# Optimization experiments

Measured on AMD Instinct MI355X. Metric: run time of the kernel, lower is better.

Reference implementation:

```python
import itertools
import jax, jax.numpy as jnp
import numpy as np

TAU = 1e-06


def build_A_system(M: int) -> np.ndarray:
    """All binary matrices A in {0,1}^{2 x M} with exactly one 1 per column,
    excluding the two assignments where one group is empty. Shape [K, 2, M],
    K = 2^M - 2."""
    mats = []
    for assign in itertools.product([0, 1], repeat=M):
        s = sum(assign)
        if s == 0 or s == M:
            continue
        A = np.zeros((2, M), dtype=np.float32)
        for i, val in enumerate(assign):
            A[val, i] = 1.0
        mats.append(A)
    return np.stack(mats, axis=0)


def setup_inputs() -> dict:
    key = jax.random.key(0)
    k1, k2 = jax.random.split(key)
    B, M, T = 8, 8, 32000
    estimated_sources = jax.random.normal(k1, (B, M, T), dtype=jnp.float32)
    input_mixtures = jax.random.normal(k2, (B, 2, T), dtype=jnp.float32)
    return {"estimated_sources": estimated_sources, "input_mixtures": input_mixtures}


def reference(estimated_sources, input_mixtures):
    B, M, T = estimated_sources.shape
    assert input_mixtures.shape[1] == 2
    # [K, 2, M] binary assignment matrices (static, built at trace time)
    A = jnp.asarray(build_A_system(M), dtype=estimated_sources.dtype)
    # Remix estimated sources under every assignment: [B, K, 2, T]
    est = jnp.einsum('kjm,bmt->bkjt', A, estimated_sources)
    # Per-mixture input energy: [B, 2]
    input_energy = jnp.sum(input_mixtures ** 2, axis=-1)
    # Noise energy per (batch, combo, mixture): [B, K, 2]
    noise_energy = jnp.sum((input_mixtures[:, None, :, :] - est) ** 2, axis=-1)
    ie = input_energy[:, None, :]  # [B, 1, 2] broadcast over K
    # Negative SNR in dB: [B, K, 2]
    snr_loss = -10.0 * jnp.log10(ie / (noise_energy + TAU * ie))
    # Sum over the two mixtures, minimize over assignments, mean over batch
    per_combo = jnp.sum(snr_loss, axis=-1)     # [B, K]
    per_sample = jnp.min(per_combo, axis=-1)   # [B]
    return jnp.mean(per_sample)
```

## Files before the change

kernel.cpp:

```cpp
#include <hip/hip_runtime.h>
#include <math.h>

#define TAU 1e-6f

constexpr int Mm = 8;
constexpr int Bb = 8;
constexpr int Tt = 32000;
constexpr int NCOL = Tt / 4;
constexpr int BLKS_PER_B = 32;
constexpr int NBLK = BLKS_PER_B * Bb;
constexpr int NSTAT = 54;
constexpr int WS_STRIDE = 64;

#define STAT_LIST(X) \
  X(e0,0) X(e1,1) \
  X(c00,2) X(c01,3) X(c02,4) X(c03,5) X(c04,6) X(c05,7) X(c06,8) X(c07,9) \
  X(c10,10) X(c11,11) X(c12,12) X(c13,13) X(c14,14) X(c15,15) X(c16,16) X(c17,17) \
  X(g00,18) X(g01,19) X(g02,20) X(g03,21) X(g04,22) X(g05,23) X(g06,24) X(g07,25) \
  X(g11,26) X(g12,27) X(g13,28) X(g14,29) X(g15,30) X(g16,31) X(g17,32) \
  X(g22,33) X(g23,34) X(g24,35) X(g25,36) X(g26,37) X(g27,38) \
  X(g33,39) X(g34,40) X(g35,41) X(g36,42) X(g37,43) \
  X(g44,44) X(g45,45) X(g46,46) X(g47,47) \
  X(g55,48) X(g56,49) X(g57,50) \
  X(g66,51) X(g67,52) \
  X(g77,53)

#define DECL_STAT(v,i) float v = 0.0f;

#define COMP_UPDATE(F) do { \
  const float x0 = x0v.F, x1 = x1v.F; \
  const float t0 = s0v.F, t1 = s1v.F, t2 = s2v.F, t3 = s3v.F; \
  const float t4 = s4v.F, t5 = s5v.F, t6 = s6v.F, t7 = s7v.F; \
  e0 = fmaf(x0, x0, e0);  e1 = fmaf(x1, x1, e1); \
  c00 = fmaf(x0, t0, c00); c01 = fmaf(x0, t1, c01); c02 = fmaf(x0, t2, c02); c03 = fmaf(x0, t3, c03); \
  c04 = fmaf(x0, t4, c04); c05 = fmaf(x0, t5, c05); c06 = fmaf(x0, t6, c06); c07 = fmaf(x0, t7, c07); \
  c10 = fmaf(x1, t0, c10); c11 = fmaf(x1, t1, c11); c12 = fmaf(x1, t2, c12); c13 = fmaf(x1, t3, c13); \
  c14 = fmaf(x1, t4, c14); c15 = fmaf(x1, t5, c15); c16 = fmaf(x1, t6, c16); c17 = fmaf(x1, t7, c17); \
  g00 = fmaf(t0, t0, g00); g01 = fmaf(t0, t1, g01); g02 = fmaf(t0, t2, g02); g03 = fmaf(t0, t3, g03); \
  g04 = fmaf(t0, t4, g04); g05 = fmaf(t0, t5, g05); g06 = fmaf(t0, t6, g06); g07 = fmaf(t0, t7, g07); \
  g11 = fmaf(t1, t1, g11); g12 = fmaf(t1, t2, g12); g13 = fmaf(t1, t3, g13); g14 = fmaf(t1, t4, g14); \
  g15 = fmaf(t1, t5, g15); g16 = fmaf(t1, t6, g16); g17 = fmaf(t1, t7, g17); \
  g22 = fmaf(t2, t2, g22); g23 = fmaf(t2, t3, g23); g24 = fmaf(t2, t4, g24); g25 = fmaf(t2, t5, g25); \
  g26 = fmaf(t2, t6, g26); g27 = fmaf(t2, t7, g27); \
  g33 = fmaf(t3, t3, g33); g34 = fmaf(t3, t4, g34); g35 = fmaf(t3, t5, g35); g36 = fmaf(t3, t6, g36); \
  g37 = fmaf(t3, t7, g37); \
  g44 = fmaf(t4, t4, g44); g45 = fmaf(t4, t5, g45); g46 = fmaf(t4, t6, g46); g47 = fmaf(t4, t7, g47); \
  g55 = fmaf(t5, t5, g55); g56 = fmaf(t5, t6, g56); g57 = fmaf(t5, t7, g57); \
  g66 = fmaf(t6, t6, g66); g67 = fmaf(t6, t7, g67); \
  g77 = fmaf(t7, t7, g77); \
} while (0)

#define REDUCE_STORE(v,i) { \
  float r_ = v; \
  r_ += __shfl_down(r_, 32, 64); r_ += __shfl_down(r_, 16, 64); \
  r_ += __shfl_down(r_, 8, 64);  r_ += __shfl_down(r_, 4, 64); \
  r_ += __shfl_down(r_, 2, 64);  r_ += __shfl_down(r_, 1, 64); \
  if (lane == 0) sh[wv][i] = r_; \
}

__global__ void __launch_bounds__(256, 1) mixit_reduce_kernel(
    const float* __restrict__ es,
    const float* __restrict__ im,
    float* __restrict__ ws) {
    const int tid = threadIdx.x;
    const int b   = blockIdx.x >> 5;
    const int blk = blockIdx.x & 31;
    const int col = blk * 256 + tid;

    STAT_LIST(DECL_STAT)

    if (col < NCOL) {
        const float4* esb4 = (const float4*)(es + (size_t)b * Mm * Tt);
        const float4* imb4 = (const float4*)(im + (size_t)b * 2 * Tt);
        const float4 x0v = imb4[col];
        const float4 x1v = imb4[NCOL + col];
        const float4 s0v = esb4[0 * NCOL + col];
        const float4 s1v = esb4[1 * NCOL + col];
        const float4 s2v = esb4[2 * NCOL + col];
        const float4 s3v = esb4[3 * NCOL + col];
        const float4 s4v = esb4[4 * NCOL + col];
        const float4 s5v = esb4[5 * NCOL + col];
        const float4 s6v = esb4[6 * NCOL + col];
        const float4 s7v = esb4[7 * NCOL + col];
        COMP_UPDATE(x);
        COMP_UPDATE(y);
        COMP_UPDATE(z);
        COMP_UPDATE(w);
    }

    __shared__ float sh[4][NSTAT];
    {
        const int lane = tid & 63;
        const int wv   = tid >> 6;
        STAT_LIST(REDUCE_STORE)
    }
    __syncthreads();
    if (tid < NSTAT) {
        ws[(size_t)blockIdx.x * WS_STRIDE + tid] =
            sh[0][tid] + sh[1][tid] + sh[2][tid] + sh[3][tid];
    }
}

__global__ void __launch_bounds__(512) mixit_finalize_kernel(
    const float* __restrict__ ws,
    float* __restrict__ out) {
    __shared__ float stats[Bb][NSTAT];
    __shared__ float minb[Bb];
    const int tid = threadIdx.x;

    if (tid < Bb * NSTAT) {
        const int bb = tid / NSTAT, s = tid - bb * NSTAT;
        const float* base = ws + (size_t)bb * BLKS_PER_B * WS_STRIDE + s;
        float acc = 0.0f;
#pragma unroll
        for (int k = 0; k < BLKS_PER_B; ++k) acc += base[k * WS_STRIDE];
        stats[bb][s] = acc;
    }
    __syncthreads();

    const int wv   = tid >> 6;
    const int lane = tid & 63;
    const float* st = stats[wv];
    const float E0 = st[0];
    const float E1 = st[1];

    float qmin = INFINITY;
#pragma unroll 1
    for (int ci = 0; ci < 4; ++ci) {
        const int cm1 = lane + (ci << 6);
        if (cm1 < 254) {
            const int c = cm1 + 1;
            float ne0 = E0;
            float ne1 = E1;
#pragma unroll
            for (int m = 0; m < Mm; ++m) {
                if ((c >> m) & 1) ne1 -= 2.0f * st[10 + m];
                else              ne0 -= 2.0f * st[2 + m];
            }
            int p = 18;
#pragma unroll
            for (int m = 0; m < Mm; ++m) {
#pragma unroll
                for (int mp = m; mp < Mm; ++mp, ++p) {
                    const float g = st[p];
                    const float w = (m == mp) ? 1.0f : 2.0f;
                    const int bm  = (c >> m) & 1;
                    const int bmp = (c >> mp) & 1;
                    if (bm & bmp)         ne1 += w * g;
                    else if (!(bm | bmp)) ne0 += w * g;
                }
            }
            qmin = fminf(qmin, (ne0 + TAU * E0) * (ne1 + TAU * E1));
        }
    }
#pragma unroll
    for (int off = 32; off > 0; off >>= 1)
        qmin = fminf(qmin, __shfl_down(qmin, off, 64));
    if (lane == 0) minb[wv] = 10.0f * log10f(qmin / (E0 * E1));
    __syncthreads();

    if (tid == 0) {
        float tot = 0.0f;
#pragma unroll
        for (int i = 0; i < Bb; ++i) tot += minb[i];
        out[0] = tot / (float)Bb;
    }
}

extern "C" void kernel_launch(void* const* d_in, const int* in_sizes, int n_in,
                              void* d_out, int out_size, void* d_ws, size_t ws_size,
                              hipStream_t stream) {
    const float* es = (const float*)d_in[0];
    const float* im = (const float*)d_in[1];
    float* out = (float*)d_out;
    float* ws  = (float*)d_ws;

    mixit_reduce_kernel<<<dim3(NBLK), dim3(256), 0, stream>>>(es, im, ws);
    mixit_finalize_kernel<<<1, 512, 0, stream>>>(ws, out);
}
```

Measured before the change: 29.34 us.

## Fuse reduce and finalize kernels via atomics and last-block completion counter

Replaces the two-kernel pipeline with a single kernel. Each block atomically adds its partial statistics into a per-batch accumulator, and the last block to increment a global counter runs the finalize step. A memset is added to zero the accumulators. This removes the second kernel launch and its dependency gap, at the cost of atomic contention, a memset node, and order-dependent float summation.

```diff
diff --git a/kernel.cpp b/kernel.cpp
--- a/kernel.cpp
+++ b/kernel.cpp
@@ -10,7 +10,8 @@
 constexpr int BLKS_PER_B = 32;
 constexpr int NBLK = BLKS_PER_B * Bb;
 constexpr int NSTAT = 54;
-constexpr int WS_STRIDE = 64;
+constexpr int GS_STRIDE = 64;
+constexpr int CTR_OFF = Bb * GS_STRIDE;
 
 #define STAT_LIST(X) \
   X(e0,0) X(e1,1) \
@@ -58,10 +59,11 @@
   if (lane == 0) sh[wv][i] = r_; \
 }
 
-__global__ void __launch_bounds__(256, 1) mixit_reduce_kernel(
+__global__ void __launch_bounds__(256, 1) mixit_fused_kernel(
     const float* __restrict__ es,
     const float* __restrict__ im,
-    float* __restrict__ ws) {
+    float* __restrict__ ws,
+    float* __restrict__ out) {
     const int tid = threadIdx.x;
     const int b   = blockIdx.x >> 5;
     const int blk = blockIdx.x & 31;
@@ -89,74 +91,83 @@
     }
 
     __shared__ float sh[4][NSTAT];
+    __shared__ int is_last;
     {
         const int lane = tid & 63;
         const int wv   = tid >> 6;
         STAT_LIST(REDUCE_STORE)
     }
     __syncthreads();
+
     if (tid < NSTAT) {
-        ws[(size_t)blockIdx.x * WS_STRIDE + tid] =
-            sh[0][tid] + sh[1][tid] + sh[2][tid] + sh[3][tid];
+        const float p = sh[0][tid] + sh[1][tid] + sh[2][tid] + sh[3][tid];
+        const float old = atomicAdd(&ws[(size_t)b * GS_STRIDE + tid], p);
+        asm volatile("" :: "v"(old));
     }
-}
+    __syncthreads();
 
-__global__ void __launch_bounds__(512) mixit_finalize_kernel(
-    const float* __restrict__ ws,
-    float* __restrict__ out) {
+    if (tid == 0) {
+        const int t = atomicAdd((int*)(ws + CTR_OFF), 1);
+        is_last = (t == NBLK - 1);
+    }
+    __syncthreads();
+    if (!is_last) return;
+
     __shared__ float stats[Bb][NSTAT];
     __shared__ float minb[Bb];
-    const int tid = threadIdx.x;
 
-    if (tid < Bb * NSTAT) {
-        const int bb = tid / NSTAT, s = tid - bb * NSTAT;
-        const float* base = ws + (size_t)bb * BLKS_PER_B * WS_STRIDE + s;
-        float acc = 0.0f;
-#pragma unroll
-        for (int k = 0; k < BLKS_PER_B; ++k) acc += base[k * WS_STRIDE];
-        stats[bb][s] = acc;
+    for (int i = tid; i < Bb * NSTAT; i += 256) {
+        const int bb = i / NSTAT, s = i - bb * NSTAT;
+        stats[bb][s] = __hip_atomic_load(&ws[(size_t)bb * GS_STRIDE + s],
+                                         __ATOMIC_RELAXED,
+                                         __HIP_MEMORY_SCOPE_AGENT);
     }
     __syncthreads();
 
     const int wv   = tid >> 6;
     const int lane = tid & 63;
-    const float* st = stats[wv];
-    const float E0 = st[0];
-    const float E1 = st[1];
 
-    float qmin = INFINITY;
 #pragma unroll 1
-    for (int ci = 0; ci < 4; ++ci) {
-        const int cm1 = lane + (ci << 6);
-        if (cm1 < 254) {
-            const int c = cm1 + 1;
-            float ne0 = E0;
-            float ne1 = E1;
+    for (int rep = 0; rep < 2; ++rep) {
+        const int bb = wv + 4 * rep;
+        const float* st = stats[bb];
+        const float E0 = st[0];
+        const float E1 = st[1];
+
+        float qmin = INFINITY;
+#pragma unroll 1
+        for (int ci = 0; ci < 4; ++ci) {
+            const int cm1 = lane + (ci << 6);
+            if (cm1 < 254) {
+                const int c = cm1 + 1;
+                float ne0 = E0;
+                float ne1 = E1;
 #pragma unroll
-            for (int m = 0; m < Mm; ++m) {
-                if ((c >> m) & 1) ne1 -= 2.0f * st[10 + m];
-                else              ne0 -= 2.0f * st[2 + m];
+                for (int m = 0; m < Mm; ++m) {
+                    if ((c >> m) & 1) ne1 -= 2.0f * st[10 + m];
+                    else              ne0 -= 2.0f * st[2 + m];
+                }
+                int p = 18;
+#pragma unroll
+                for (int m = 0; m < Mm; ++m) {
+#pragma unroll
+                    for (int mp = m; mp < Mm; ++mp, ++p) {
+                        const float g = st[p];
+                        const float w = (m == mp) ? 1.0f : 2.0f;
+                        const int bm  = (c >> m) & 1;
+                        const int bmp = (c >> mp) & 1;
+                        if (bm & bmp)         ne1 += w * g;
+                        else if (!(bm | bmp)) ne0 += w * g;
+                    }
+                }
+                qmin = fminf(qmin, (ne0 + TAU * E0) * (ne1 + TAU * E1));
             }
-            int p = 18;
+        }
 #pragma unroll
-            for (int m = 0; m < Mm; ++m) {
-#pragma unroll
-                for (int mp = m; mp < Mm; ++mp, ++p) {
-                    const float g = st[p];
-                    const float w = (m == mp) ? 1.0f : 2.0f;
-                    const int bm  = (c >> m) & 1;
-                    const int bmp = (c >> mp) & 1;
-                    if (bm & bmp)         ne1 += w * g;
-                    else if (!(bm | bmp)) ne0 += w * g;
-                }
-            }
-            qmin = fminf(qmin, (ne0 + TAU * E0) * (ne1 + TAU * E1));
-        }
+        for (int off = 32; off > 0; off >>= 1)
+            qmin = fminf(qmin, __shfl_down(qmin, off, 64));
+        if (lane == 0) minb[bb] = 10.0f * log10f(qmin / (E0 * E1));
     }
-#pragma unroll
-    for (int off = 32; off > 0; off >>= 1)
-        qmin = fminf(qmin, __shfl_down(qmin, off, 64));
-    if (lane == 0) minb[wv] = 10.0f * log10f(qmin / (E0 * E1));
     __syncthreads();
 
     if (tid == 0) {
@@ -175,6 +186,7 @@
     float* out = (float*)d_out;
     float* ws  = (float*)d_ws;
 
-    mixit_reduce_kernel<<<dim3(NBLK), dim3(256), 0, stream>>>(es, im, ws);
-    mixit_finalize_kernel<<<1, 512, 0, stream>>>(ws, out);
+    hipMemsetAsync(ws, 0, (CTR_OFF + 1) * sizeof(float), stream);
+
+    mixit_fused_kernel<<<dim3(NBLK), dim3(256), 0, stream>>>(es, im, ws, out);
 }
```

New measurement: 47.09 us. 60.5% more time.
